# Kernel tuning notes

Measured on AMD Instinct MI355X. Metric: run time of the kernel, lower is better.

The kernel has to match this reference:

```python
import jax, jax.numpy as jnp
import numpy as np
import math

DIM = 384
HEADS = 6
HEAD_DIM = DIM // HEADS
MLP_HIDDEN = int(DIM * 2.0)


def layer_norm(x, g, b, eps=1e-5):
    mu = jnp.mean(x, axis=-1, keepdims=True)
    var = jnp.mean((x - mu) ** 2, axis=-1, keepdims=True)
    return (x - mu) * jax.lax.rsqrt(var + eps) * g + b


def setup_inputs() -> dict:
    key = jax.random.key(0)
    ks = jax.random.split(key, 12)
    B, N = 4, 2048
    s = 0.02
    return {
        "x": jax.random.normal(ks[0], (B, N, DIM), dtype=jnp.float32),
        "pos": jax.random.normal(ks[1], (B, N, 3), dtype=jnp.float32),
        "qkv_w": jax.random.normal(ks[2], (DIM, 3 * DIM), dtype=jnp.float32) * s,
        "qkv_b": jnp.zeros((3 * DIM,), jnp.float32),
        "proj_w": jax.random.normal(ks[3], (DIM, DIM), dtype=jnp.float32) * s,
        "proj_b": jnp.zeros((DIM,), jnp.float32),
        "mlp_w1": jax.random.normal(ks[4], (DIM, MLP_HIDDEN), dtype=jnp.float32) * s,
        "mlp_b1": jnp.zeros((MLP_HIDDEN,), jnp.float32),
        "mlp_w2": jax.random.normal(ks[5], (MLP_HIDDEN, DIM), dtype=jnp.float32) * s,
        "mlp_b2": jnp.zeros((DIM,), jnp.float32),
        "ln1_g": jnp.ones((DIM,), jnp.float32),
        "ln1_b": jnp.zeros((DIM,), jnp.float32),
        "ln2_g": jnp.ones((DIM,), jnp.float32),
        "ln2_b": jnp.zeros((DIM,), jnp.float32),
    }


def reference(x, pos, qkv_w, qkv_b, proj_w, proj_b, mlp_w1, mlp_b1,
              mlp_w2, mlp_b2, ln1_g, ln1_b, ln2_g, ln2_b):
    B, N, D = x.shape
    H, Hd = HEADS, HEAD_DIM
    # qkv projection
    qkv = layer_norm(x, ln1_g, ln1_b) @ qkv_w + qkv_b          # [B,N,3D]
    qkv = qkv.reshape(B, N, 3, H, Hd)
    q = jnp.transpose(qkv[:, :, 0], (0, 2, 1, 3))               # [B,H,N,Hd]
    k = jnp.transpose(qkv[:, :, 1], (0, 2, 1, 3))
    v = jnp.transpose(qkv[:, :, 2], (0, 2, 1, 3))
    # pairwise squared-distance bias: exp(-||p_i - p_j||^2)
    rel = pos[:, :, None, :] - pos[:, None, :, :]               # [B,N,N,3]
    dist = jnp.exp(-jnp.sum(rel ** 2, axis=-1))                 # [B,N,N]
    scale = 1.0 / math.sqrt(Hd)
    attn = jnp.einsum('bhqd,bhkd->bhqk', q, k) * scale + dist[:, None, :, :]
    attn = jax.nn.softmax(attn, axis=-1)
    out = jnp.einsum('bhqk,bhkd->bhqd', attn, v)                # [B,H,N,Hd]
    out = jnp.transpose(out, (0, 2, 1, 3)).reshape(B, N, D)
    out = out @ proj_w + proj_b
    x = x + out
    h = layer_norm(x, ln2_g, ln2_b)
    h = jax.nn.gelu(h @ mlp_w1 + mlp_b1, approximate=False) @ mlp_w2 + mlp_b2
    return x + h
```

## Files before the change

### kernel.cpp

```cpp
#include <hip/hip_runtime.h>
#include <hip/hip_bf16.h>
#include <math.h>

#define DIMD 384
#define NHEADS 6
#define HD 64
#define MLPH 768
#define SEQ 2048
#define NBATCH 4
#define NTOK (NBATCH*SEQ)

typedef __hip_bfloat16 bf16;

typedef __attribute__((ext_vector_type(8))) short bf16x8;
typedef __attribute__((ext_vector_type(4))) float f32x4;

#define LOG2E 1.44269504088896340736f

static __device__ inline float fexp2(float x) { return __builtin_amdgcn_exp2f(x); }

static __device__ inline f32x4 mfma16(bf16x8 a, bf16x8 b, f32x4 c) {
    return __builtin_amdgcn_mfma_f32_16x16x32_bf16(a, b, c, 0, 0, 0);
}

static __device__ inline unsigned int cvtpk(float lo, float hi) {
    unsigned int r;
    asm("v_cvt_pk_bf16_f32 %0, %1, %2" : "=v"(r) : "v"(lo), "v"(hi));
    return r;
}
static __device__ inline float bflo(unsigned int u) { return __builtin_bit_cast(float, u << 16); }
static __device__ inline float bfhi(unsigned int u) { return __builtin_bit_cast(float, u & 0xffff0000u); }

static __device__ inline void gld16(const void* g, void* l) {
    __builtin_amdgcn_global_load_lds(
        (const __attribute__((address_space(1))) unsigned int*)g,
        (__attribute__((address_space(3))) unsigned int*)l, 16, 0, 0);
}

static __device__ inline int xcd_swz(int wg, int nwg) {
    return (wg & 7) * (nwg >> 3) + (wg >> 3);
}

__global__ __launch_bounds__(256) void ln_k(const float* __restrict__ x,
                                            const float* __restrict__ gm,
                                            const float* __restrict__ bt,
                                            bf16* __restrict__ out) {
    int row = blockIdx.x * 4 + (threadIdx.x >> 6);
    int l = threadIdx.x & 63;
    const float* xr = x + (size_t)row * DIMD;
    float v[6];
#pragma unroll
    for (int j = 0; j < 6; ++j) v[j] = xr[l + 64 * j];
    float s = 0.f, s2 = 0.f;
#pragma unroll
    for (int j = 0; j < 6; ++j) { s += v[j]; s2 += v[j] * v[j]; }
#pragma unroll
    for (int m = 1; m < 64; m <<= 1) { s += __shfl_xor(s, m); s2 += __shfl_xor(s2, m); }
    float mu = s * (1.f / DIMD);
    float var = s2 * (1.f / DIMD) - mu * mu;
    float rs = rsqrtf(var + 1e-5f);
    bf16* orow = out + (size_t)row * DIMD;
#pragma unroll
    for (int j = 0; j < 6; ++j) {
        int i = l + 64 * j;
        orow[i] = __float2bfloat16((v[j] - mu) * rs * gm[i] + bt[i]);
    }
}

__global__ __launch_bounds__(256) void prep_k(const float* __restrict__ w1,
                                              const float* __restrict__ w2,
                                              const float* __restrict__ w3,
                                              const float* __restrict__ w4,
                                              bf16* __restrict__ o1,
                                              bf16* __restrict__ o2,
                                              bf16* __restrict__ o3,
                                              bf16* __restrict__ o4,
                                              const float* __restrict__ pos,
                                              bf16* __restrict__ DP,
                                              const float* __restrict__ x,
                                              const float* __restrict__ g1,
                                              const float* __restrict__ b1,
                                              bf16* __restrict__ xn) {
    __shared__ float t[32][33];
    int id = blockIdx.x;
    if (id < 1152) {
        const float* W; bf16* O; int K, N;
        if (id < 432)      { W = w1; O = o1; K = 384; N = 1152; }
        else if (id < 576) { W = w2; O = o2; K = 384; N = 384;  id -= 432; }
        else if (id < 864) { W = w3; O = o3; K = 384; N = 768;  id -= 576; }
        else               { W = w4; O = o4; K = 768; N = 384;  id -= 864; }
        int nbx = N >> 5;
        int nb = (id % nbx) * 32, kb = (id / nbx) * 32;
        int tx = threadIdx.x & 31, ty = threadIdx.x >> 5;
#pragma unroll
        for (int i = 0; i < 4; ++i)
            t[ty + 8 * i][tx] = W[(size_t)(kb + ty + 8 * i) * N + nb + tx];
        __syncthreads();
#pragma unroll
        for (int i = 0; i < 4; ++i)
            O[(size_t)(nb + ty + 8 * i) * K + kb + tx] = __float2bfloat16(t[tx][ty + 8 * i]);
    } else if (id < 1664) {
        int blk = id - 1152;
        int w = blk & 3, qt = (blk >> 2) & 31, b = blk >> 7;
        int l = threadIdx.x & 63, tt = threadIdx.x >> 6;
        int lq = l & 15, g = l >> 4;
        int q = qt * 64 + w * 16 + lq;
        const float* pq = pos + ((size_t)b * SEQ + q) * 3;
        float px = pq[0], py = pq[1], pz = pq[2];
        const float* posb = pos + (size_t)b * SEQ * 3;
        char* base = (char*)DP + (size_t)blk * 65536;
        for (int j = 0; j < 8; ++j) {
            int tt8 = tt * 8 + j;
#pragma unroll
            for (int m = 0; m < 2; ++m) {
                int k0 = tt8 * 64 + 32 * m + 4 * g;
                float a[24];
                const float* pk = posb + 3 * k0;
                *(f32x4*)&a[0]  = *(const f32x4*)pk;
                *(f32x4*)&a[4]  = *(const f32x4*)(pk + 4);
                *(f32x4*)&a[8]  = *(const f32x4*)(pk + 8);
                const float* pk2 = posb + 3 * (k0 + 16);
                *(f32x4*)&a[12] = *(const f32x4*)pk2;
                *(f32x4*)&a[16] = *(const f32x4*)(pk2 + 4);
                *(f32x4*)&a[20] = *(const f32x4*)(pk2 + 8);
                float o8[8];
#pragma unroll
                for (int r = 0; r < 8; ++r) {
                    float dx = px - a[3 * r], dy = py - a[3 * r + 1], dz = pz - a[3 * r + 2];
                    o8[r] = fexp2(-LOG2E * (dx * dx + dy * dy + dz * dz)) * LOG2E;
                }
                uint4 o;
                o.x = cvtpk(o8[0], o8[1]); o.y = cvtpk(o8[2], o8[3]);
                o.z = cvtpk(o8[4], o8[5]); o.w = cvtpk(o8[6], o8[7]);
                *(uint4*)(base + ((size_t)tt8 * 2 + m) * 1024 + l * 16) = o;
            }
        }
    } else {
        int row = (id - 1664) * 4 + (threadIdx.x >> 6);
        int l = threadIdx.x & 63;
        const float* xr = x + (size_t)row * DIMD;
        float v[6];
#pragma unroll
        for (int j = 0; j < 6; ++j) v[j] = xr[l + 64 * j];
        float s = 0.f, s2 = 0.f;
#pragma unroll
        for (int j = 0; j < 6; ++j) { s += v[j]; s2 += v[j] * v[j]; }
#pragma unroll
        for (int m = 1; m < 64; m <<= 1) { s += __shfl_xor(s, m); s2 += __shfl_xor(s2, m); }
        float mu = s * (1.f / DIMD);
        float var = s2 * (1.f / DIMD) - mu * mu;
        float rs = rsqrtf(var + 1e-5f);
        bf16* orow = xn + (size_t)row * DIMD;
#pragma unroll
        for (int j = 0; j < 6; ++j) {
            int i = l + 64 * j;
            orow[i] = __float2bfloat16((v[j] - mu) * rs * g1[i] + b1[i]);
        }
    }
}

template <int EPI, int NX>
__global__ __launch_bounds__(256) void gemm128_k(const bf16* __restrict__ A,
                                                 const bf16* __restrict__ WT,
                                                 const float* __restrict__ bias,
                                                 bf16* __restrict__ ob0,
                                                 bf16* __restrict__ ob1,
                                                 bf16* __restrict__ ob2,
                                                 int K, int Nw) {
    __shared__ __align__(16) char Als[2][8192];
    __shared__ __align__(16) char Bls[2][8192];
    int tid = threadIdx.x;
    int w = tid >> 6, l = tid & 63;
    int c = l & 15, g = l >> 4;
    int wr = w >> 1, wc = w & 1;
    int swz = xcd_swz(blockIdx.x, gridDim.x);
    int m0 = (swz / NX) * 128, n0 = (swz % NX) * 128;
    const char* Ag = (const char*)A + (size_t)m0 * K * 2;
    const char* Bg = (const char*)WT + (size_t)n0 * K * 2;
    int K2 = K * 2;

    f32x4 acc[4][4];
#pragma unroll
    for (int mi = 0; mi < 4; ++mi)
#pragma unroll
        for (int ni = 0; ni < 4; ++ni) acc[mi][ni] = (f32x4){0.f, 0.f, 0.f, 0.f};

    auto stage = [&](int t, int bi) {
#pragma unroll
        for (int p = 0; p < 2; ++p) {
            int chunk = p * 256 + tid;
            int r = chunk >> 2;
            int cc = ((chunk & 3) ^ (r & 3)) << 4;
            gld16(Ag + (size_t)r * K2 + t * 64 + cc, &Als[bi][chunk * 16]);
            gld16(Bg + (size_t)r * K2 + t * 64 + cc, &Bls[bi][chunk * 16]);
        }
    };

    stage(0, 0);
    int kcn = K >> 5;
    for (int t = 0; t < kcn; ++t) {
        int bi = t & 1;
        __syncthreads();
        if (t + 1 < kcn) stage(t + 1, bi ^ 1);
        bf16x8 af[4], bfr[4];
#pragma unroll
        for (int mi = 0; mi < 4; ++mi) {
            int row = wr * 64 + mi * 16 + c;
            __builtin_memcpy(&af[mi], &Als[bi][row * 64 + ((g ^ (row & 3)) << 4)], 16);
        }
#pragma unroll
        for (int ni = 0; ni < 4; ++ni) {
            int row = wc * 64 + ni * 16 + c;
            __builtin_memcpy(&bfr[ni], &Bls[bi][row * 64 + ((g ^ (row & 3)) << 4)], 16);
        }
#pragma unroll
        for (int mi = 0; mi < 4; ++mi)
#pragma unroll
            for (int ni = 0; ni < 4; ++ni)
                acc[mi][ni] = mfma16(af[mi], bfr[ni], acc[mi][ni]);
    }

#pragma unroll
    for (int mi = 0; mi < 4; ++mi) {
#pragma unroll
        for (int ni = 0; ni < 4; ++ni) {
            int ntb = n0 + wc * 64 + ni * 16;
#pragma unroll
            for (int r = 0; r < 4; ++r) {
                int m = m0 + wr * 64 + mi * 16 + 4 * g + r;
                int n = ntb + c;
                float val = acc[mi][ni][r] + bias[n];
                if (EPI == 0) {
                    int which = ntb / DIMD;
                    int rem = ntb - which * DIMD;
                    int h = rem >> 6;
                    int d = (rem & 63) + c;
                    int b = m >> 11, s = m & (SEQ - 1);
                    if (which == 2) {
                        int slot = (s & ~31) + 8 * ((m & 15) >> 2) + 4 * ((m >> 4) & 1) + (m & 3);
                        ob2[(((size_t)b * NHEADS + h) * HD + d) * SEQ + slot] = __float2bfloat16(val);
                    } else {
                        bf16* dp = which == 0 ? ob0 : ob1;
                        dp[(((size_t)b * NHEADS + h) * SEQ + s) * HD + d] = __float2bfloat16(val);
                    }
                } else {
                    float ge = 0.5f * val * (1.0f + erff(val * 0.70710678118654752f));
                    ob0[(size_t)m * Nw + n] = __float2bfloat16(ge);
                }
            }
        }
    }
}

template <int NX>
__global__ __launch_bounds__(256) void gemm_k(const bf16* __restrict__ A,
                                              const bf16* __restrict__ WT,
                                              const float* __restrict__ bias,
                                              const float* __restrict__ resid,
                                              float* __restrict__ outf,
                                              int K, int Nw) {
    __shared__ __align__(16) char Als[2][8192];
    __shared__ __align__(16) char Bls[2][8192];
    int tid = threadIdx.x;
    int w = tid >> 6, l = tid & 63;
    int c = l & 15, g = l >> 4;
    int swz = xcd_swz(blockIdx.x, gridDim.x);
    int m0 = (swz / NX) * 64, n0 = (swz % NX) * 64;
    const char* Ag = (const char*)A + (size_t)m0 * K * 2;
    const char* Bg = (const char*)WT + (size_t)n0 * K * 2;
    int K2 = K * 2;

    f32x4 acc[4];
#pragma unroll
    for (int nt = 0; nt < 4; ++nt) acc[nt] = (f32x4){0.f, 0.f, 0.f, 0.f};

    auto stage = [&](int t, int bi) {
#pragma unroll
        for (int p = 0; p < 2; ++p) {
            int chunk = p * 256 + tid;
            int r = chunk >> 3;
            int cc = ((chunk & 7) ^ (r & 7)) << 4;
            gld16(Ag + (size_t)r * K2 + t * 128 + cc, &Als[bi][chunk * 16]);
            gld16(Bg + (size_t)r * K2 + t * 128 + cc, &Bls[bi][chunk * 16]);
        }
    };

    stage(0, 0);
    int kcn = K >> 6;
    int arow = (16 * w + c) * 128;
    int sw = c & 7;
    for (int t = 0; t < kcn; ++t) {
        int bi = t & 1;
        __syncthreads();
        if (t + 1 < kcn) stage(t + 1, bi ^ 1);
#pragma unroll
        for (int kk = 0; kk < 2; ++kk) {
            int ch = ((kk * 4 + g) ^ sw) << 4;
            bf16x8 af;
            __builtin_memcpy(&af, &Als[bi][arow + ch], 16);
#pragma unroll
            for (int nt = 0; nt < 4; ++nt) {
                bf16x8 bfr;
                __builtin_memcpy(&bfr, &Bls[bi][(nt * 16 + c) * 128 + ch], 16);
                acc[nt] = mfma16(af, bfr, acc[nt]);
            }
        }
    }

#pragma unroll
    for (int nt = 0; nt < 4; ++nt) {
        int ntb = n0 + nt * 16;
#pragma unroll
        for (int r = 0; r < 4; ++r) {
            int m = m0 + 16 * w + 4 * g + r;
            int n = ntb + c;
            float val = acc[nt][r] + bias[n];
            val += resid[(size_t)m * Nw + n];
            outf[(size_t)m * Nw + n] = val;
        }
    }
}

__global__ __launch_bounds__(256) void attn_k(const bf16* __restrict__ q,
                                              const bf16* __restrict__ k,
                                              const bf16* __restrict__ vT,
                                              const bf16* __restrict__ DP,
                                              bf16* __restrict__ out) {
    __shared__ __align__(16) char Kls[3][8192];
    __shared__ __align__(16) char Vls[3][8192];

    int tid = threadIdx.x;
    int w = tid >> 6, l = tid & 63;
    int lq = l & 15, g = l >> 4;
    int swzb = xcd_swz(blockIdx.x, gridDim.x);
    int qt = swzb & 31;
    int bh = swzb >> 5;
    int b = bh / NHEADS, h = bh % NHEADS;
    int qrow = qt * 64 + w * 16 + lq;

    const bf16* qp = q + ((size_t)bh * SEQ + qrow) * HD + 8 * g;
    bf16x8 qf0 = *(const bf16x8*)qp;
    bf16x8 qf1 = *(const bf16x8*)(qp + 32);

    const char* kgb = (const char*)(k + (size_t)bh * SEQ * HD);
    const char* vgb = (const char*)(vT + (size_t)bh * HD * SEQ);
    const char* dpb = (const char*)DP + ((size_t)((b * 32 + qt) * 4 + w)) * 65536 + l * 16;

    const float SC2 = 0.125f * LOG2E;
    f32x4 oacc[4];
#pragma unroll
    for (int dt = 0; dt < 4; ++dt) oacc[dt] = (f32x4){0.f, 0.f, 0.f, 0.f};
    f32x4 osum = (f32x4){0.f, 0.f, 0.f, 0.f};
    bf16x8 ones = {(short)0x3F80, (short)0x3F80, (short)0x3F80, (short)0x3F80,
                   (short)0x3F80, (short)0x3F80, (short)0x3F80, (short)0x3F80};

    int swq = lq & 7;
    int offA = lq * 128 + ((g ^ swq) << 4);
    int offB = lq * 128 + (((4 + g) ^ swq) << 4);

    auto stage = [&](int t, int B2) {
#pragma unroll
        for (int p = 0; p < 2; ++p) {
            int chunk = p * 256 + tid;
            int r = chunk >> 3, c = chunk & 7;
            int cc = (c ^ (r & 7)) << 4;
            gld16(kgb + (size_t)t * 8192 + r * 128 + cc, &Kls[B2][chunk * 16]);
            gld16(vgb + (size_t)r * 4096 + t * 128 + cc, &Vls[B2][chunk * 16]);
        }
    };

    stage(0, 0);
    uint4 cdp0 = *(const uint4*)(dpb);
    uint4 cdp1 = *(const uint4*)(dpb + 1024);
    stage(1, 1);

    auto body = [&](int t, int B0, int B2) {
        asm volatile("s_waitcnt vmcnt(4)" ::: "memory");
        __builtin_amdgcn_sched_barrier(0);
        __builtin_amdgcn_s_barrier();
        __builtin_amdgcn_sched_barrier(0);

        const char* Kb = &Kls[B0][0];
        const char* Vb = &Vls[B0][0];
        f32x4 st[4];
        __builtin_amdgcn_s_setprio(1);
#pragma unroll
        for (int s = 0; s < 4; ++s) {
            bf16x8 klo, khi;
            __builtin_memcpy(&klo, Kb + s * 2048 + offA, 16);
            __builtin_memcpy(&khi, Kb + s * 2048 + offB, 16);
            f32x4 z = (f32x4){0.f, 0.f, 0.f, 0.f};
            st[s] = mfma16(klo, qf0, z);
            st[s] = mfma16(khi, qf1, st[s]);
        }
        __builtin_amdgcn_s_setprio(0);

#pragma unroll
        for (int m = 0; m < 2; ++m) {
            uint4 cd = m == 0 ? cdp0 : cdp1;
            int offV = m == 0 ? offA : offB;
            f32x4 s0v = st[2 * m], s1v = st[2 * m + 1];
            float p[8];
            p[0] = fexp2(s0v[0] * SC2 + bflo(cd.x));
            p[1] = fexp2(s0v[1] * SC2 + bfhi(cd.x));
            p[2] = fexp2(s0v[2] * SC2 + bflo(cd.y));
            p[3] = fexp2(s0v[3] * SC2 + bfhi(cd.y));
            p[4] = fexp2(s1v[0] * SC2 + bflo(cd.z));
            p[5] = fexp2(s1v[1] * SC2 + bfhi(cd.z));
            p[6] = fexp2(s1v[2] * SC2 + bflo(cd.w));
            p[7] = fexp2(s1v[3] * SC2 + bfhi(cd.w));

            unsigned int pw[4];
            pw[0] = cvtpk(p[0], p[1]);
            pw[1] = cvtpk(p[2], p[3]);
            pw[2] = cvtpk(p[4], p[5]);
            pw[3] = cvtpk(p[6], p[7]);
            bf16x8 pf;
            __builtin_memcpy(&pf, pw, 16);

            __builtin_amdgcn_s_setprio(1);
            osum = mfma16(ones, pf, osum);
#pragma unroll
            for (int dt = 0; dt < 4; ++dt) {
                bf16x8 vf;
                __builtin_memcpy(&vf, Vb + dt * 2048 + offV, 16);
                oacc[dt] = mfma16(vf, pf, oacc[dt]);
            }
            __builtin_amdgcn_s_setprio(0);
        }

        __builtin_amdgcn_sched_barrier(0);
        int tn1 = t + 1 < 32 ? t + 1 : 31;
        const char* dpn = dpb + (size_t)tn1 * 2048;
        uint4 n0 = *(const uint4*)(dpn);
        uint4 n1 = *(const uint4*)(dpn + 1024);
        __builtin_amdgcn_sched_barrier(0);
        int tn2 = t + 2 < 32 ? t + 2 : 31;
        stage(tn2, B2);
        __builtin_amdgcn_sched_barrier(0);
        cdp0 = n0; cdp1 = n1;
    };

    for (int t = 0; t < 30; t += 3) {
        body(t + 0, 0, 2);
        body(t + 1, 1, 0);
        body(t + 2, 2, 1);
    }
    body(30, 0, 2);
    body(31, 1, 0);

    float inv = 1.f / osum[0];
    bf16* op = out + ((size_t)b * SEQ + qrow) * DIMD + h * HD + 4 * g;
#pragma unroll
    for (int dt = 0; dt < 4; ++dt) {
        unsigned int t2[2];
        t2[0] = cvtpk(oacc[dt][0] * inv, oacc[dt][1] * inv);
        t2[1] = cvtpk(oacc[dt][2] * inv, oacc[dt][3] * inv);
        __builtin_memcpy(op + dt * 16, t2, 8);
    }
}

extern "C" void kernel_launch(void* const* d_in, const int* in_sizes, int n_in,
                              void* d_out, int out_size, void* d_ws, size_t ws_size,
                              hipStream_t stream) {
    const float* x      = (const float*)d_in[0];
    const float* pos    = (const float*)d_in[1];
    const float* qkv_w  = (const float*)d_in[2];
    const float* qkv_b  = (const float*)d_in[3];
    const float* proj_w = (const float*)d_in[4];
    const float* proj_b = (const float*)d_in[5];
    const float* mlp_w1 = (const float*)d_in[6];
    const float* mlp_b1 = (const float*)d_in[7];
    const float* mlp_w2 = (const float*)d_in[8];
    const float* mlp_b2 = (const float*)d_in[9];
    const float* ln1_g  = (const float*)d_in[10];
    const float* ln1_b  = (const float*)d_in[11];
    const float* ln2_g  = (const float*)d_in[12];
    const float* ln2_b  = (const float*)d_in[13];

    char* p = (char*)d_ws;
    size_t off = 0;
    auto alloc = [&](size_t bytes) {
        char* r = p + off;
        off = (off + bytes + 255) & ~(size_t)255;
        return r;
    };
    bf16* WT1 = (bf16*)alloc((size_t)1152 * 384 * 2);
    bf16* WT2 = (bf16*)alloc((size_t)384 * 384 * 2);
    bf16* WT3 = (bf16*)alloc((size_t)384 * 768 * 2);
    bf16* WT4 = (bf16*)alloc((size_t)768 * 384 * 2);
    bf16* xn  = (bf16*)alloc((size_t)NTOK * DIMD * 2);
    bf16* xn2 = (bf16*)alloc((size_t)NTOK * DIMD * 2);
    bf16* qb  = (bf16*)alloc((size_t)NTOK * DIMD * 2);
    bf16* kb  = (bf16*)alloc((size_t)NTOK * DIMD * 2);
    bf16* vTb = (bf16*)alloc((size_t)NTOK * DIMD * 2);
    bf16* ao  = (bf16*)alloc((size_t)NTOK * DIMD * 2);
    float* x1 = (float*)alloc((size_t)NTOK * DIMD * 4);
    bf16* hh  = (bf16*)alloc((size_t)NTOK * MLPH * 2);
    bf16* dtab = (bf16*)alloc((size_t)NBATCH * SEQ * SEQ * 2);
    if (off > ws_size) return;

    prep_k<<<1152 + 512 + 2048, 256, 0, stream>>>(
        qkv_w, proj_w, mlp_w1, mlp_w2, WT1, WT2, WT3, WT4,
        pos, dtab, x, ln1_g, ln1_b, xn);

    gemm128_k<0, 9><<<576, 256, 0, stream>>>(
        xn, WT1, qkv_b, qb, kb, vTb, 384, 1152);
    attn_k<<<NBATCH * NHEADS * (SEQ / 64), 256, 0, stream>>>(qb, kb, vTb, dtab, ao);
    gemm_k<6><<<768, 256, 0, stream>>>(
        ao, WT2, proj_b, x, x1, 384, 384);
    ln_k<<<NTOK / 4, 256, 0, stream>>>(x1, ln2_g, ln2_b, xn2);
    gemm128_k<2, 6><<<384, 256, 0, stream>>>(
        xn2, WT3, mlp_b1, hh, nullptr, nullptr, 384, 768);
    gemm_k<6><<<768, 256, 0, stream>>>(
        hh, WT4, mlp_b2, x1, (float*)d_out, 768, 384);
}
```

Measured before the change: 129.3 us.

## Fold softmax scale into Q and bias into MFMA accumulator; stage pos in LDS

Q is pre-scaled by 0.125*log2e in the QKV GEMM epilogue, and the bf16 distance bias is fed as the initial MFMA accumulator. This removes the per-element multiply-add before exp2 in the attention inner loop. Separately, the distance-bias precompute stages each batch's positions into shared memory instead of reading them from global memory per tile. Rounding the pre-scaled Q to bf16 slightly changes precision, and the prep kernel now uses a larger shared buffer that may lower occupancy.

```diff
diff --git a/kernel.cpp b/kernel.cpp
--- a/kernel.cpp
+++ b/kernel.cpp
@@ -16,6 +16,7 @@
 typedef __attribute__((ext_vector_type(4))) float f32x4;
 
 #define LOG2E 1.44269504088896340736f
+#define SC2F 0.18033688011112042f
 
 static __device__ inline float fexp2(float x) { return __builtin_amdgcn_exp2f(x); }
 
@@ -81,9 +82,10 @@
                                               const float* __restrict__ g1,
                                               const float* __restrict__ b1,
                                               bf16* __restrict__ xn) {
-    __shared__ float t[32][33];
+    __shared__ float shbuf[6144];
     int id = blockIdx.x;
     if (id < 1152) {
+        float (*t)[33] = (float(*)[33])shbuf;
         const float* W; bf16* O; int K, N;
         if (id < 432)      { W = w1; O = o1; K = 384; N = 1152; }
         else if (id < 576) { W = w2; O = o2; K = 384; N = 384;  id -= 432; }
@@ -104,10 +106,12 @@
         int w = blk & 3, qt = (blk >> 2) & 31, b = blk >> 7;
         int l = threadIdx.x & 63, tt = threadIdx.x >> 6;
         int lq = l & 15, g = l >> 4;
+        const float* posb = pos + (size_t)b * SEQ * 3;
+        for (int i = threadIdx.x; i < 1536; i += 256)
+            ((f32x4*)shbuf)[i] = ((const f32x4*)posb)[i];
+        __syncthreads();
         int q = qt * 64 + w * 16 + lq;
-        const float* pq = pos + ((size_t)b * SEQ + q) * 3;
-        float px = pq[0], py = pq[1], pz = pq[2];
-        const float* posb = pos + (size_t)b * SEQ * 3;
+        float px = shbuf[3 * q], py = shbuf[3 * q + 1], pz = shbuf[3 * q + 2];
         char* base = (char*)DP + (size_t)blk * 65536;
         for (int j = 0; j < 8; ++j) {
             int tt8 = tt * 8 + j;
@@ -115,14 +119,12 @@
             for (int m = 0; m < 2; ++m) {
                 int k0 = tt8 * 64 + 32 * m + 4 * g;
                 float a[24];
-                const float* pk = posb + 3 * k0;
-                *(f32x4*)&a[0]  = *(const f32x4*)pk;
-                *(f32x4*)&a[4]  = *(const f32x4*)(pk + 4);
-                *(f32x4*)&a[8]  = *(const f32x4*)(pk + 8);
-                const float* pk2 = posb + 3 * (k0 + 16);
-                *(f32x4*)&a[12] = *(const f32x4*)pk2;
-                *(f32x4*)&a[16] = *(const f32x4*)(pk2 + 4);
-                *(f32x4*)&a[20] = *(const f32x4*)(pk2 + 8);
+                *(f32x4*)&a[0]  = *(const f32x4*)&shbuf[3 * k0];
+                *(f32x4*)&a[4]  = *(const f32x4*)&shbuf[3 * k0 + 4];
+                *(f32x4*)&a[8]  = *(const f32x4*)&shbuf[3 * k0 + 8];
+                *(f32x4*)&a[12] = *(const f32x4*)&shbuf[3 * (k0 + 16)];
+                *(f32x4*)&a[16] = *(const f32x4*)&shbuf[3 * (k0 + 16) + 4];
+                *(f32x4*)&a[20] = *(const f32x4*)&shbuf[3 * (k0 + 16) + 8];
                 float o8[8];
 #pragma unroll
                 for (int r = 0; r < 8; ++r) {
@@ -240,6 +242,7 @@
                         int slot = (s & ~31) + 8 * ((m & 15) >> 2) + 4 * ((m >> 4) & 1) + (m & 3);
                         ob2[(((size_t)b * NHEADS + h) * HD + d) * SEQ + slot] = __float2bfloat16(val);
                     } else {
+                        if (which == 0) val *= SC2F;
                         bf16* dp = which == 0 ? ob0 : ob1;
                         dp[(((size_t)b * NHEADS + h) * SEQ + s) * HD + d] = __float2bfloat16(val);
                     }
@@ -346,7 +349,6 @@
     const char* vgb = (const char*)(vT + (size_t)bh * HD * SEQ);
     const char* dpb = (const char*)DP + ((size_t)((b * 32 + qt) * 4 + w)) * 65536 + l * 16;
 
-    const float SC2 = 0.125f * LOG2E;
     f32x4 oacc[4];
 #pragma unroll
     for (int dt = 0; dt < 4; ++dt) oacc[dt] = (f32x4){0.f, 0.f, 0.f, 0.f};
@@ -382,6 +384,11 @@
 
         const char* Kb = &Kls[B0][0];
         const char* Vb = &Vls[B0][0];
+        f32x4 bc[4];
+        bc[0] = (f32x4){bflo(cdp0.x), bfhi(cdp0.x), bflo(cdp0.y), bfhi(cdp0.y)};
+        bc[1] = (f32x4){bflo(cdp0.z), bfhi(cdp0.z), bflo(cdp0.w), bfhi(cdp0.w)};
+        bc[2] = (f32x4){bflo(cdp1.x), bfhi(cdp1.x), bflo(cdp1.y), bfhi(cdp1.y)};
+        bc[3] = (f32x4){bflo(cdp1.z), bfhi(cdp1.z), bflo(cdp1.w), bfhi(cdp1.w)};
         f32x4 st[4];
         __builtin_amdgcn_s_setprio(1);
 #pragma unroll
@@ -389,26 +396,24 @@
             bf16x8 klo, khi;
             __builtin_memcpy(&klo, Kb + s * 2048 + offA, 16);
             __builtin_memcpy(&khi, Kb + s * 2048 + offB, 16);
-            f32x4 z = (f32x4){0.f, 0.f, 0.f, 0.f};
-            st[s] = mfma16(klo, qf0, z);
+            st[s] = mfma16(klo, qf0, bc[s]);
             st[s] = mfma16(khi, qf1, st[s]);
         }
         __builtin_amdgcn_s_setprio(0);
 
 #pragma unroll
         for (int m = 0; m < 2; ++m) {
-            uint4 cd = m == 0 ? cdp0 : cdp1;
             int offV = m == 0 ? offA : offB;
             f32x4 s0v = st[2 * m], s1v = st[2 * m + 1];
             float p[8];
-            p[0] = fexp2(s0v[0] * SC2 + bflo(cd.x));
-            p[1] = fexp2(s0v[1] * SC2 + bfhi(cd.x));
-            p[2] = fexp2(s0v[2] * SC2 + bflo(cd.y));
-            p[3] = fexp2(s0v[3] * SC2 + bfhi(cd.y));
-            p[4] = fexp2(s1v[0] * SC2 + bflo(cd.z));
-            p[5] = fexp2(s1v[1] * SC2 + bfhi(cd.z));
-            p[6] = fexp2(s1v[2] * SC2 + bflo(cd.w));
-            p[7] = fexp2(s1v[3] * SC2 + bfhi(cd.w));
+            p[0] = fexp2(s0v[0]);
+            p[1] = fexp2(s0v[1]);
+            p[2] = fexp2(s0v[2]);
+            p[3] = fexp2(s0v[3]);
+            p[4] = fexp2(s1v[0]);
+            p[5] = fexp2(s1v[1]);
+            p[6] = fexp2(s1v[2]);
+            p[7] = fexp2(s1v[3]);
 
             unsigned int pw[4];
             pw[0] = cvtpk(p[0], p[1]);
```

Result: no change. 129.6 us (+0.2%).
